# Kernel tuning notes

Hardware: AMD Instinct MI355X
Metric: run time of the kernel (lower is better)

The kernel has to match this reference:

```python
import jax, jax.numpy as jnp
import numpy as np

N_FFT = 800
HOP = 200
WIN = 800
FREQ = N_FFT // 2 + 1  # 401
B, T = 32, 480000


def _make_weights():
    # periodic hann window
    n = np.arange(N_FFT)
    window = 0.5 - 0.5 * np.cos(2.0 * np.pi * np.arange(WIN) / WIN)
    k = np.arange(FREQ)
    angle = 2.0 * np.pi * np.outer(k, n) / N_FFT  # [FREQ, N_FFT]
    fwd_real = (np.cos(angle) * window).astype(np.float32)
    fwd_imag = (-np.sin(angle) * window).astype(np.float32)
    angle_t = 2.0 * np.pi * np.outer(n, k) / N_FFT  # [N_FFT, FREQ]
    inv_window = window * (1.0 / N_FFT)
    bwd_real = (np.cos(angle_t).T * inv_window).astype(np.float32)  # [FREQ, N_FFT]
    bwd_imag = (np.sin(angle_t).T * inv_window).astype(np.float32)
    return (jnp.asarray(fwd_real), jnp.asarray(fwd_imag),
            jnp.asarray(bwd_real), jnp.asarray(bwd_imag))


def setup_inputs() -> dict:
    key = jax.random.key(0)
    x = jax.random.normal(key, (B, T), dtype=jnp.float32)
    wfr, wfi, wbr, wbi = _make_weights()
    return {"x": x, "w_fwd_real": wfr, "w_fwd_imag": wfi,
            "w_bwd_real": wbr, "w_bwd_imag": wbi}


def reference(x, w_fwd_real, w_fwd_imag, w_bwd_real, w_bwd_imag):
    Tlen = x.shape[-1]
    pad = N_FFT // 2
    xp = jnp.pad(x, ((0, 0), (pad, pad)), mode="edge")  # replicate pad
    n_frames = (xp.shape[-1] - N_FFT) // HOP + 1
    # frame extraction (== conv1d stride HOP with dense DFT kernels)
    fidx = jnp.arange(n_frames)[:, None] * HOP + jnp.arange(N_FFT)[None, :]
    frames = xp[:, fidx]  # [B, F, N_FFT]
    real = jnp.einsum("bfn,kn->bkf", frames, w_fwd_real)  # [B, FREQ, F]
    imag = jnp.einsum("bfn,kn->bkf", frames, w_fwd_imag)
    magnitude = jnp.sqrt(real * real + imag * imag + 1e-14)
    phase = jnp.arctan2(imag, real)
    phase = jnp.where((imag == 0) & (real < 0), jnp.pi, phase)
    # inverse: iDFT-as-GEMM + overlap-add (== conv_transpose1d stride HOP)
    rp = magnitude * jnp.cos(phase)
    ip = magnitude * jnp.sin(phase)
    yr = jnp.einsum("bkf,kn->bfn", rp, w_bwd_real)  # [B, F, N_FFT]
    yi = jnp.einsum("bkf,kn->bfn", ip, w_bwd_imag)
    y_frames = yr - yi
    l_out = (n_frames - 1) * HOP + N_FFT
    oidx = jnp.arange(n_frames)[:, None] * HOP + jnp.arange(N_FFT)[None, :]
    wave = jnp.zeros((x.shape[0], l_out), dtype=x.dtype).at[:, oidx].add(y_frames)
    return wave[:, pad:pad + Tlen]
```

## Files before the change

kernel.cpp:

```cpp
#include <hip/hip_runtime.h>
#include <math.h>

#define HOP     200
#define NB      32
#define TLEN    480000
#define SEG     60
#define NTILE   (TLEN / HOP / SEG)
#define NSEGP   (SEG + 6)

#define DLT  0.00785398163397448f
#define C1K  0.99996915760f
#define S1K  0.00785390090f
#define C2K  0.99987663248f
#define S2K  0.01570731731f
#define C3K  0.99972243010f
#define S3K  0.02355976470f
#define C40  0.95105651629515f
#define S40  0.30901699437495f

typedef float floatx4 __attribute__((ext_vector_type(4)));

__global__ __launch_bounds__(256) void stft_tile(const float* __restrict__ x,
                                                 float* __restrict__ out) {
    __shared__ float  part[NSEGP][10][6];
    __shared__ float  pg[NSEGP][6];
    __shared__ float4 segc[2][SEG];

    const int qb = blockIdx.x;
    const int b  = blockIdx.y;
    const int q0 = qb * SEG;
    const float* xb = x + (size_t)b * TLEN;

    for (int u = threadIdx.x; u < NSEGP * 10; u += 256) {
        const int s = u / 10;
        const int k = u - 10 * s;
        const int g = q0 - 3 + s;
        const int gm = (g + 4) & 3;
        float c0, sn0;
        __sincosf((float)(gm * 200 + 4 * k) * DLT, &sn0, &c0);
        float p1e = 0.f, p1o = 0.f, pce = 0.f, pco = 0.f, pse = 0.f, pso = 0.f;
        const bool inb = (g >= 0) && (g <= 2399);
        float4 ve;
        if (!inb) {
            const float xe = (g < 0) ? xb[0] : xb[TLEN - 1];
            ve = make_float4(xe, xe, xe, xe);
        }
#pragma unroll
        for (int i = 0; i < 5; ++i) {
            float4 v;
            if (inb) v = ((const float4*)(xb + 200 * g))[k + 10 * i];
            else     v = ve;
            const float c1 = c0 * C1K - sn0 * S1K, s1 = sn0 * C1K + c0 * S1K;
            const float c2 = c0 * C2K - sn0 * S2K, s2 = sn0 * C2K + c0 * S2K;
            const float c3 = c0 * C3K - sn0 * S3K, s3 = sn0 * C3K + c0 * S3K;
            p1e += v.x + v.z;             p1o += v.y + v.w;
            pce += c0 * v.x + c2 * v.z;   pco += c1 * v.y + c3 * v.w;
            pse += sn0 * v.x + s2 * v.z;  pso += s1 * v.y + s3 * v.w;
            const float cn = c0 * C40 - sn0 * S40;
            sn0 = sn0 * C40 + c0 * S40;  c0 = cn;
        }
        part[s][k][0] = p1e;  part[s][k][1] = p1o;
        part[s][k][2] = pce;  part[s][k][3] = pco;
        part[s][k][4] = pse;  part[s][k][5] = pso;
    }
    __syncthreads();

    for (int u = threadIdx.x; u < NSEGP * 6; u += 256) {
        const int s = u / 6;
        const int c = u - 6 * s;
        float a = 0.f;
#pragma unroll
        for (int k = 0; k < 10; ++k) a += part[s][k][c];
        pg[s][c] = a;
    }
    __syncthreads();

    if (threadIdx.x < 2 * SEG) {
        const int par = threadIdx.x & 1;
        const int ql  = threadIdx.x >> 1;
        const int q   = q0 + ql;
        float A = 0.f, C = 0.f, D = 0.f;
#pragma unroll
        for (int df = -1; df <= 2; ++df) {
            const int f = q + df;
            if (f < 0 || f > 2400) continue;
            const int ls0 = f - q0 + 1;
            float sp1 = 0.f, spc = 0.f, sps = 0.f;
#pragma unroll
            for (int kk = 0; kk < 4; ++kk) {
                const float* rec = pg[ls0 + kk];
                sp1 += rec[par];  spc += rec[2 + par];  sps += rec[4 + par];
            }
            const int fm = f & 3;
            const float tr = (fm == 0) ? spc : (fm == 1) ? sps : (fm == 2) ? -spc : -sps;
            const float S = 0.5f * sp1 + 0.5f * tr;
            A += S;
            if (fm == 0) C += S; else if (fm == 2) C -= S;
            else if (fm == 1) D += S; else D -= S;
        }
        segc[par][ql] = make_float4(A * (1.0f / 1600.0f),
                                    sqrtf(C * C + D * D) * (1.0f / 1600.0f),
                                    atan2f(D, C), 0.f);
    }
    __syncthreads();

    const bool headblk = (qb == 0);
    const bool tailblk = (qb == NTILE - 1);
    const float4* xg4 = (const float4*)(xb + HOP * q0);
    floatx4* og4 = (floatx4*)(out + (size_t)b * TLEN + HOP * q0);
    const int pmb = (q0 & 3) * 200 + 400;
    for (int j = threadIdx.x; j < 50 * SEG; j += 256) {
        const float4 xv = xg4[j];
        const int sl = j / 50;
        const float4 ce = segc[0][sl];
        const float4 co = segc[1][sl];
        const int pm = (pmb + 4 * j) % 800;
        const float xa[4] = {xv.x, xv.y, xv.z, xv.w};
        float r[4];
#pragma unroll
        for (int c = 0; c < 4; ++c) {
            const float4 cc = (c & 1) ? co : ce;
            r[c] = 0.75f * xa[c] + cc.x - cc.y * __cosf((float)(pm + c) * DLT - cc.z);
        }
        if (headblk && sl == 0) {
#pragma unroll
            for (int c = 0; c < 4; ++c) {
                const float wm = 0.5f + 0.5f * __sinf((float)(pm + c) * DLT);
                r[c] -= 0.5f * wm * wm * xa[c];
            }
        }
        if (tailblk && sl == SEG - 1) {
#pragma unroll
            for (int c = 0; c < 4; ++c) {
                const float wm = 0.5f - 0.5f * __sinf((float)(pm + c) * DLT);
                r[c] -= 0.5f * wm * wm * xa[c];
            }
        }
        floatx4 rv = {r[0], r[1], r[2], r[3]};
        __builtin_nontemporal_store(rv, &og4[j]);
    }
}

extern "C" void kernel_launch(void* const* d_in, const int* in_sizes, int n_in,
                              void* d_out, int out_size, void* d_ws, size_t ws_size,
                              hipStream_t stream) {
    const float* x = (const float*)d_in[0];
    float* out = (float*)d_out;
    stft_tile<<<dim3(NTILE, NB), dim3(256), 0, stream>>>(x, out);
}
```

Baseline: 121.0 us.

## Split fused STFT tile kernel into partial-sum and synthesis kernels via workspace

Splits the single fused kernel into two. The first computes per-segment partial DFT sums once and writes them to a global workspace. The second reads the halo rows from that workspace and runs the synthesis pass. This removes the redundant recomputation of the 6 halo segments per tile and the x re-reads they cost. In exchange it adds a second launch and a small global round trip. The fused kernel stays as a fallback when no workspace is available.

```diff
diff --git a/kernel.cpp b/kernel.cpp
--- a/kernel.cpp
+++ b/kernel.cpp
@@ -4,6 +4,14 @@
 #define HOP     200
 #define NB      32
 #define TLEN    480000
+#define NROWS   2440
+
+#define NSEG1   40
+#define NBLK1   61
+
+#define SEGO    40
+#define NT2     60
+
 #define SEG     60
 #define NTILE   (TLEN / HOP / SEG)
 #define NSEGP   (SEG + 6)
@@ -19,6 +27,138 @@
 #define S40  0.30901699437495f
 
 typedef float floatx4 __attribute__((ext_vector_type(4)));
+
+__global__ __launch_bounds__(256) void stft_part(const float* __restrict__ x,
+                                                 float* __restrict__ pg) {
+    __shared__ float part[NSEG1][10][6];
+    const int b  = blockIdx.y;
+    const int s0 = blockIdx.x * NSEG1;
+    const float* xb = x + (size_t)b * TLEN;
+
+    for (int u = threadIdx.x; u < NSEG1 * 10; u += 256) {
+        const int s = u / 10;
+        const int k = u - 10 * s;
+        const int g = s0 + s - 3;
+        const int gm = (g + 4) & 3;
+        float c0, sn0;
+        __sincosf((float)(gm * 200 + 4 * k) * DLT, &sn0, &c0);
+        float p1e = 0.f, p1o = 0.f, pce = 0.f, pco = 0.f, pse = 0.f, pso = 0.f;
+        const bool inb = (g >= 0) && (g <= 2399);
+        float4 ve;
+        if (!inb) {
+            const float xe = (g < 0) ? xb[0] : xb[TLEN - 1];
+            ve = make_float4(xe, xe, xe, xe);
+        }
+#pragma unroll
+        for (int i = 0; i < 5; ++i) {
+            float4 v;
+            if (inb) v = ((const float4*)(xb + 200 * g))[k + 10 * i];
+            else     v = ve;
+            const float c1 = c0 * C1K - sn0 * S1K, s1 = sn0 * C1K + c0 * S1K;
+            const float c2 = c0 * C2K - sn0 * S2K, s2 = sn0 * C2K + c0 * S2K;
+            const float c3 = c0 * C3K - sn0 * S3K, s3 = sn0 * C3K + c0 * S3K;
+            p1e += v.x + v.z;             p1o += v.y + v.w;
+            pce += c0 * v.x + c2 * v.z;   pco += c1 * v.y + c3 * v.w;
+            pse += sn0 * v.x + s2 * v.z;  pso += s1 * v.y + s3 * v.w;
+            const float cn = c0 * C40 - sn0 * S40;
+            sn0 = sn0 * C40 + c0 * S40;  c0 = cn;
+        }
+        part[s][k][0] = p1e;  part[s][k][1] = p1o;
+        part[s][k][2] = pce;  part[s][k][3] = pco;
+        part[s][k][4] = pse;  part[s][k][5] = pso;
+    }
+    __syncthreads();
+
+    for (int u = threadIdx.x; u < NSEG1 * 6; u += 256) {
+        const int s = u / 6;
+        const int c = u - 6 * s;
+        float a = 0.f;
+#pragma unroll
+        for (int k = 0; k < 10; ++k) a += part[s][k][c];
+        pg[((size_t)b * NROWS + s0 + s) * 6 + c] = a;
+    }
+}
+
+__global__ __launch_bounds__(256) void stft_synth(const float* __restrict__ x,
+                                                  const float* __restrict__ pg,
+                                                  float* __restrict__ out) {
+    __shared__ float  pgs[SEGO + 6][6];
+    __shared__ float4 segc[2][SEGO];
+    const int qb = blockIdx.x;
+    const int b  = blockIdx.y;
+    const int q0 = qb * SEGO;
+    const float* xb = x + (size_t)b * TLEN;
+
+    const float* pgb = pg + ((size_t)b * NROWS + q0) * 6;
+    for (int u = threadIdx.x; u < (SEGO + 6) * 6; u += 256)
+        ((float*)pgs)[u] = pgb[u];
+    __syncthreads();
+
+    if (threadIdx.x < 2 * SEGO) {
+        const int par = threadIdx.x & 1;
+        const int ql  = threadIdx.x >> 1;
+        const int q   = q0 + ql;
+        float A = 0.f, C = 0.f, D = 0.f;
+#pragma unroll
+        for (int df = -1; df <= 2; ++df) {
+            const int f = q + df;
+            if (f < 0 || f > 2400) continue;
+            const int ls0 = f - q0 + 1;
+            float sp1 = 0.f, spc = 0.f, sps = 0.f;
+#pragma unroll
+            for (int kk = 0; kk < 4; ++kk) {
+                const float* rec = pgs[ls0 + kk];
+                sp1 += rec[par];  spc += rec[2 + par];  sps += rec[4 + par];
+            }
+            const int fm = f & 3;
+            const float tr = (fm == 0) ? spc : (fm == 1) ? sps : (fm == 2) ? -spc : -sps;
+            const float S = 0.5f * sp1 + 0.5f * tr;
+            A += S;
+            if (fm == 0) C += S; else if (fm == 2) C -= S;
+            else if (fm == 1) D += S; else D -= S;
+        }
+        segc[par][ql] = make_float4(A * (1.0f / 1600.0f),
+                                    sqrtf(C * C + D * D) * (1.0f / 1600.0f),
+                                    atan2f(D, C), 0.f);
+    }
+    __syncthreads();
+
+    const bool headblk = (qb == 0);
+    const bool tailblk = (qb == NT2 - 1);
+    const float4* xg4 = (const float4*)(xb + HOP * q0);
+    floatx4* og4 = (floatx4*)(out + (size_t)b * TLEN + HOP * q0);
+    const int pmb = (q0 & 3) * 200 + 400;
+    for (int j = threadIdx.x; j < 50 * SEGO; j += 256) {
+        const float4 xv = xg4[j];
+        const int sl = j / 50;
+        const float4 ce = segc[0][sl];
+        const float4 co = segc[1][sl];
+        const int pm = (pmb + 4 * j) % 800;
+        const float xa[4] = {xv.x, xv.y, xv.z, xv.w};
+        float r[4];
+#pragma unroll
+        for (int c = 0; c < 4; ++c) {
+            const float4 cc = (c & 1) ? co : ce;
+            r[c] = 0.75f * xa[c] + cc.x - cc.y * __cosf((float)(pm + c) * DLT - cc.z);
+        }
+        if (headblk && sl == 0) {
+#pragma unroll
+            for (int c = 0; c < 4; ++c) {
+                const float wm = 0.5f + 0.5f * __sinf((float)(pm + c) * DLT);
+                r[c] -= 0.5f * wm * wm * xa[c];
+            }
+        }
+        if (tailblk && sl == SEGO - 1) {
+#pragma unroll
+            for (int c = 0; c < 4; ++c) {
+                const float wm = 0.5f - 0.5f * __sinf((float)(pm + c) * DLT);
+                r[c] -= 0.5f * wm * wm * xa[c];
+            }
+        }
+        floatx4 rv = {r[0], r[1], r[2], r[3]};
+        __builtin_nontemporal_store(rv, &og4[j]);
+    }
+}
 
 __global__ __launch_bounds__(256) void stft_tile(const float* __restrict__ x,
                                                  float* __restrict__ out) {
@@ -146,5 +286,12 @@
                               hipStream_t stream) {
     const float* x = (const float*)d_in[0];
     float* out = (float*)d_out;
-    stft_tile<<<dim3(NTILE, NB), dim3(256), 0, stream>>>(x, out);
-}
+    const size_t need = (size_t)NB * NROWS * 6 * sizeof(float);
+    if (d_ws != nullptr && ws_size >= need) {
+        float* pg = (float*)d_ws;
+        stft_part<<<dim3(NBLK1, NB), dim3(256), 0, stream>>>(x, pg);
+        stft_synth<<<dim3(NT2, NB), dim3(256), 0, stream>>>(x, pg, out);
+    } else {
+        stft_tile<<<dim3(NTILE, NB), dim3(256), 0, stream>>>(x, out);
+    }
+}
```

Result: slower. 127.9 us (+5.7%).

## Stage input window in LDS and shrink tile to 20 segments

Applied to the files above, without the earlier changes.

The block's input window, including the three-segment halos on each side, is now loaded once from global memory into shared memory with coalesced float4 loads. Both the partial-DFT pass and the final output pass read it from there instead of re-reading global memory. The tile size drops from 60 to 20 hops, which triples the grid and raises occupancy. The cost is relatively more halo traffic per tile (6 extra segments per 20) and an extra barrier.

```diff
diff --git a/kernel.cpp b/kernel.cpp
--- a/kernel.cpp
+++ b/kernel.cpp
@@ -4,9 +4,12 @@
 #define HOP     200
 #define NB      32
 #define TLEN    480000
-#define SEG     60
+#define TLEN4   (TLEN / 4)
+#define SEG     20
 #define NTILE   (TLEN / HOP / SEG)
 #define NSEGP   (SEG + 6)
+#define NW4     (50 * NSEGP)
+#define DOFF    150
 
 #define DLT  0.00785398163397448f
 #define C1K  0.99996915760f
@@ -22,6 +25,7 @@
 
 __global__ __launch_bounds__(256) void stft_tile(const float* __restrict__ x,
                                                  float* __restrict__ out) {
+    __shared__ float4 xw4[NW4];
     __shared__ float  part[NSEGP][10][6];
     __shared__ float  pg[NSEGP][6];
     __shared__ float4 segc[2][SEG];
@@ -30,6 +34,34 @@
     const int b  = blockIdx.y;
     const int q0 = qb * SEG;
     const float* xb = x + (size_t)b * TLEN;
+    const float4* xg = (const float4*)xb;
+
+    {
+        const int jg0 = 50 * (q0 - 3);
+        float4 r[6];
+#pragma unroll
+        for (int i = 0; i < 6; ++i) {
+            const int j = threadIdx.x + 256 * i;
+            if (j < NW4) {
+                const int jg = jg0 + j;
+                if (jg < 0) {
+                    const float e = xb[0];
+                    r[i] = make_float4(e, e, e, e);
+                } else if (jg >= TLEN4) {
+                    const float e = xb[TLEN - 1];
+                    r[i] = make_float4(e, e, e, e);
+                } else {
+                    r[i] = xg[jg];
+                }
+            }
+        }
+#pragma unroll
+        for (int i = 0; i < 6; ++i) {
+            const int j = threadIdx.x + 256 * i;
+            if (j < NW4) xw4[j] = r[i];
+        }
+    }
+    __syncthreads();
 
     for (int u = threadIdx.x; u < NSEGP * 10; u += 256) {
         const int s = u / 10;
@@ -38,24 +70,20 @@
         const int gm = (g + 4) & 3;
         float c0, sn0;
         __sincosf((float)(gm * 200 + 4 * k) * DLT, &sn0, &c0);
+
+        float4 v[5];
+#pragma unroll
+        for (int i = 0; i < 5; ++i) v[i] = xw4[50 * s + k + 10 * i];
+
         float p1e = 0.f, p1o = 0.f, pce = 0.f, pco = 0.f, pse = 0.f, pso = 0.f;
-        const bool inb = (g >= 0) && (g <= 2399);
-        float4 ve;
-        if (!inb) {
-            const float xe = (g < 0) ? xb[0] : xb[TLEN - 1];
-            ve = make_float4(xe, xe, xe, xe);
-        }
 #pragma unroll
         for (int i = 0; i < 5; ++i) {
-            float4 v;
-            if (inb) v = ((const float4*)(xb + 200 * g))[k + 10 * i];
-            else     v = ve;
             const float c1 = c0 * C1K - sn0 * S1K, s1 = sn0 * C1K + c0 * S1K;
             const float c2 = c0 * C2K - sn0 * S2K, s2 = sn0 * C2K + c0 * S2K;
             const float c3 = c0 * C3K - sn0 * S3K, s3 = sn0 * C3K + c0 * S3K;
-            p1e += v.x + v.z;             p1o += v.y + v.w;
-            pce += c0 * v.x + c2 * v.z;   pco += c1 * v.y + c3 * v.w;
-            pse += sn0 * v.x + s2 * v.z;  pso += s1 * v.y + s3 * v.w;
+            p1e += v[i].x + v[i].z;             p1o += v[i].y + v[i].w;
+            pce += c0 * v[i].x + c2 * v[i].z;   pco += c1 * v[i].y + c3 * v[i].w;
+            pse += sn0 * v[i].x + s2 * v[i].z;  pso += s1 * v[i].y + s3 * v[i].w;
             const float cn = c0 * C40 - sn0 * S40;
             sn0 = sn0 * C40 + c0 * S40;  c0 = cn;
         }
@@ -106,11 +134,10 @@
 
     const bool headblk = (qb == 0);
     const bool tailblk = (qb == NTILE - 1);
-    const float4* xg4 = (const float4*)(xb + HOP * q0);
     floatx4* og4 = (floatx4*)(out + (size_t)b * TLEN + HOP * q0);
     const int pmb = (q0 & 3) * 200 + 400;
     for (int j = threadIdx.x; j < 50 * SEG; j += 256) {
-        const float4 xv = xg4[j];
+        const float4 xv = xw4[DOFF + j];
         const int sl = j / 50;
         const float4 ce = segc[0][sl];
         const float4 co = segc[1][sl];
```

Result: no change. 120.7 us (-0.3%).

## Make each wavefront process an independent 10-segment tile without block barriers

Applied to the files above, without the earlier changes.

Each 64-lane wavefront now owns its own tile of 10 hop segments with a private shared-memory slice, and the block barriers are replaced by an LDS waitcnt. This removes __syncthreads stalls and the idle threads in the serial per-segment phase, and the input loads are hoisted so all five float4 loads are issued before the math. The trade-off is a halo of 6 segments per 10-segment tile instead of per 60, so about 60% more redundant input reads and DFT partial work. It also relies on wavefront-synchronous execution for correctness through LDS.

```diff
diff --git a/kernel.cpp b/kernel.cpp
--- a/kernel.cpp
+++ b/kernel.cpp
@@ -4,9 +4,12 @@
 #define HOP     200
 #define NB      32
 #define TLEN    480000
-#define SEG     60
-#define NTILE   (TLEN / HOP / SEG)
-#define NSEGP   (SEG + 6)
+#define NSEGT   2400
+#define WSEG    10
+#define WPS     (WSEG + 6)
+#define NWT     (NSEGT / WSEG)
+#define WPB     4
+#define NBLKX   (NWT / WPB)
 
 #define DLT  0.00785398163397448f
 #define C1K  0.99996915760f
@@ -20,75 +23,82 @@
 
 typedef float floatx4 __attribute__((ext_vector_type(4)));
 
-__global__ __launch_bounds__(256) void stft_tile(const float* __restrict__ x,
+#define WSYNC() asm volatile("s_waitcnt lgkmcnt(0)" ::: "memory")
+
+__global__ __launch_bounds__(256) void stft_wave(const float* __restrict__ x,
                                                  float* __restrict__ out) {
-    __shared__ float  part[NSEGP][10][6];
-    __shared__ float  pg[NSEGP][6];
-    __shared__ float4 segc[2][SEG];
+    __shared__ float  part[WPB][WPS][10][6];
+    __shared__ float  pg[WPB][WPS][6];
+    __shared__ float4 segc[WPB][2][WSEG];
 
-    const int qb = blockIdx.x;
-    const int b  = blockIdx.y;
-    const int q0 = qb * SEG;
+    const int w    = threadIdx.x >> 6;
+    const int lane = threadIdx.x & 63;
+    const int b    = blockIdx.y;
+    const int wt   = blockIdx.x * WPB + w;
+    const int wq0  = wt * WSEG;
     const float* xb = x + (size_t)b * TLEN;
 
-    for (int u = threadIdx.x; u < NSEGP * 10; u += 256) {
+    for (int u = lane; u < WPS * 10; u += 64) {
         const int s = u / 10;
         const int k = u - 10 * s;
-        const int g = q0 - 3 + s;
+        const int g = wq0 - 3 + s;
         const int gm = (g + 4) & 3;
         float c0, sn0;
         __sincosf((float)(gm * 200 + 4 * k) * DLT, &sn0, &c0);
+
+        float4 v[5];
+        if (g >= 0 && g <= 2399) {
+            const float4* xs = (const float4*)(xb + 200 * g);
+#pragma unroll
+            for (int i = 0; i < 5; ++i) v[i] = xs[k + 10 * i];
+        } else {
+            const float e = (g < 0) ? xb[0] : xb[TLEN - 1];
+#pragma unroll
+            for (int i = 0; i < 5; ++i) v[i] = make_float4(e, e, e, e);
+        }
+
         float p1e = 0.f, p1o = 0.f, pce = 0.f, pco = 0.f, pse = 0.f, pso = 0.f;
-        const bool inb = (g >= 0) && (g <= 2399);
-        float4 ve;
-        if (!inb) {
-            const float xe = (g < 0) ? xb[0] : xb[TLEN - 1];
-            ve = make_float4(xe, xe, xe, xe);
-        }
 #pragma unroll
         for (int i = 0; i < 5; ++i) {
-            float4 v;
-            if (inb) v = ((const float4*)(xb + 200 * g))[k + 10 * i];
-            else     v = ve;
             const float c1 = c0 * C1K - sn0 * S1K, s1 = sn0 * C1K + c0 * S1K;
             const float c2 = c0 * C2K - sn0 * S2K, s2 = sn0 * C2K + c0 * S2K;
             const float c3 = c0 * C3K - sn0 * S3K, s3 = sn0 * C3K + c0 * S3K;
-            p1e += v.x + v.z;             p1o += v.y + v.w;
-            pce += c0 * v.x + c2 * v.z;   pco += c1 * v.y + c3 * v.w;
-            pse += sn0 * v.x + s2 * v.z;  pso += s1 * v.y + s3 * v.w;
+            p1e += v[i].x + v[i].z;             p1o += v[i].y + v[i].w;
+            pce += c0 * v[i].x + c2 * v[i].z;   pco += c1 * v[i].y + c3 * v[i].w;
+            pse += sn0 * v[i].x + s2 * v[i].z;  pso += s1 * v[i].y + s3 * v[i].w;
             const float cn = c0 * C40 - sn0 * S40;
             sn0 = sn0 * C40 + c0 * S40;  c0 = cn;
         }
-        part[s][k][0] = p1e;  part[s][k][1] = p1o;
-        part[s][k][2] = pce;  part[s][k][3] = pco;
-        part[s][k][4] = pse;  part[s][k][5] = pso;
+        part[w][s][k][0] = p1e;  part[w][s][k][1] = p1o;
+        part[w][s][k][2] = pce;  part[w][s][k][3] = pco;
+        part[w][s][k][4] = pse;  part[w][s][k][5] = pso;
     }
-    __syncthreads();
+    WSYNC();
 
-    for (int u = threadIdx.x; u < NSEGP * 6; u += 256) {
+    for (int u = lane; u < WPS * 6; u += 64) {
         const int s = u / 6;
         const int c = u - 6 * s;
         float a = 0.f;
 #pragma unroll
-        for (int k = 0; k < 10; ++k) a += part[s][k][c];
-        pg[s][c] = a;
+        for (int k = 0; k < 10; ++k) a += part[w][s][k][c];
+        pg[w][s][c] = a;
     }
-    __syncthreads();
+    WSYNC();
 
-    if (threadIdx.x < 2 * SEG) {
-        const int par = threadIdx.x & 1;
-        const int ql  = threadIdx.x >> 1;
-        const int q   = q0 + ql;
+    if (lane < 2 * WSEG) {
+        const int par = lane & 1;
+        const int ql  = lane >> 1;
+        const int q   = wq0 + ql;
         float A = 0.f, C = 0.f, D = 0.f;
 #pragma unroll
         for (int df = -1; df <= 2; ++df) {
             const int f = q + df;
             if (f < 0 || f > 2400) continue;
-            const int ls0 = f - q0 + 1;
+            const int ls0 = f - wq0 + 1;
             float sp1 = 0.f, spc = 0.f, sps = 0.f;
 #pragma unroll
             for (int kk = 0; kk < 4; ++kk) {
-                const float* rec = pg[ls0 + kk];
+                const float* rec = pg[w][ls0 + kk];
                 sp1 += rec[par];  spc += rec[2 + par];  sps += rec[4 + par];
             }
             const int fm = f & 3;
@@ -98,22 +108,22 @@
             if (fm == 0) C += S; else if (fm == 2) C -= S;
             else if (fm == 1) D += S; else D -= S;
         }
-        segc[par][ql] = make_float4(A * (1.0f / 1600.0f),
-                                    sqrtf(C * C + D * D) * (1.0f / 1600.0f),
-                                    atan2f(D, C), 0.f);
+        segc[w][par][ql] = make_float4(A * (1.0f / 1600.0f),
+                                       sqrtf(C * C + D * D) * (1.0f / 1600.0f),
+                                       atan2f(D, C), 0.f);
     }
-    __syncthreads();
+    WSYNC();
 
-    const bool headblk = (qb == 0);
-    const bool tailblk = (qb == NTILE - 1);
-    const float4* xg4 = (const float4*)(xb + HOP * q0);
-    floatx4* og4 = (floatx4*)(out + (size_t)b * TLEN + HOP * q0);
-    const int pmb = (q0 & 3) * 200 + 400;
-    for (int j = threadIdx.x; j < 50 * SEG; j += 256) {
+    const bool headw = (wq0 == 0);
+    const bool tailw = (wq0 + WSEG == NSEGT);
+    const float4* xg4 = (const float4*)xb + 50 * wq0;
+    floatx4* og4 = (floatx4*)(out + (size_t)b * TLEN) + 50 * wq0;
+    const int pmb = (wq0 & 3) * 200 + 400;
+    for (int j = lane; j < 50 * WSEG; j += 64) {
         const float4 xv = xg4[j];
         const int sl = j / 50;
-        const float4 ce = segc[0][sl];
-        const float4 co = segc[1][sl];
+        const float4 ce = segc[w][0][sl];
+        const float4 co = segc[w][1][sl];
         const int pm = (pmb + 4 * j) % 800;
         const float xa[4] = {xv.x, xv.y, xv.z, xv.w};
         float r[4];
@@ -122,14 +132,14 @@
             const float4 cc = (c & 1) ? co : ce;
             r[c] = 0.75f * xa[c] + cc.x - cc.y * __cosf((float)(pm + c) * DLT - cc.z);
         }
-        if (headblk && sl == 0) {
+        if (headw && sl == 0) {
 #pragma unroll
             for (int c = 0; c < 4; ++c) {
                 const float wm = 0.5f + 0.5f * __sinf((float)(pm + c) * DLT);
                 r[c] -= 0.5f * wm * wm * xa[c];
             }
         }
-        if (tailblk && sl == SEG - 1) {
+        if (tailw && sl == WSEG - 1) {
 #pragma unroll
             for (int c = 0; c < 4; ++c) {
                 const float wm = 0.5f - 0.5f * __sinf((float)(pm + c) * DLT);
@@ -146,5 +156,5 @@
                               hipStream_t stream) {
     const float* x = (const float*)d_in[0];
     float* out = (float*)d_out;
-    stft_tile<<<dim3(NTILE, NB), dim3(256), 0, stream>>>(x, out);
+    stft_wave<<<dim3(NBLKX, NB), dim3(256), 0, stream>>>(x, out);
 }
```

Result: slower. 128.4 us (+6.1%).
